# Kernel optimization log

Hardware: AMD Instinct MI355X
Metric: run time of the kernel (lower is better)

## Reference

```python
import jax, jax.numpy as jnp
import numpy as np

EPS_COS = 1e-8   # torch cosine_similarity denominator clamp
EPS_W = 1e-6     # min-max normalization epsilon from the module


def setup_inputs() -> dict:
    key = jax.random.key(0)
    k1, k2, k3 = jax.random.split(key, 3)
    N, D = 4096, 512
    return {
        "image_features": jax.random.normal(k1, (N, D), dtype=jnp.float32),
        "text_features": jax.random.normal(k2, (N, D), dtype=jnp.float32),
        "instr_d": jax.random.randint(k3, (N,), 0, 64, dtype=jnp.int64),
    }


def reference(image_features, text_features, instr_d):
    text_features = jax.lax.stop_gradient(text_features)  # .detach() in original
    N = image_features.shape[0]

    # per-row min-max normalized text-text similarity -> per-pair margins
    text_sim = jnp.einsum('id,jd->ij', text_features, text_features)  # [N,N]
    mn = jnp.min(text_sim, axis=1, keepdims=True)
    mx = jnp.max(text_sim, axis=1, keepdims=True)
    text_weights = (text_sim - mn) / (mx - mn + EPS_W)

    # pairwise cosine similarity image[i] vs text[j]
    img_norm = jnp.linalg.norm(image_features, axis=1)   # [N]
    txt_norm = jnp.linalg.norm(text_features, axis=1)    # [N]
    dots = jnp.einsum('id,jd->ij', image_features, text_features)
    cos = dots / jnp.maximum(img_norm[:, None] * txt_norm[None, :], EPS_COS)

    # aligned if i == j or same instruction id
    aligned = (instr_d[:, None] == instr_d[None, :]) | jnp.eye(N, dtype=bool)

    # cosine_embedding_loss: y=1 -> 1-cos ; y=-1 -> max(0, cos - margin)
    per_pair = jnp.where(aligned, 1.0 - cos, jnp.maximum(0.0, cos - text_weights))
    return jnp.mean(per_pair)
```

## Files before the change

kernel.cpp:

```cpp
#include <hip/hip_runtime.h>
#include <stdint.h>

#define NROWS 4096
#define DIM   512
#define EPS_W   1e-6f
#define NT    (NROWS / 128)
#define NKS   (DIM / 64)
#define NS    528

typedef unsigned short ushort_t;
typedef __attribute__((ext_vector_type(8))) short   short8;
typedef __attribute__((ext_vector_type(8))) unsigned short ushort8;
typedef __attribute__((ext_vector_type(4))) float   floatx4;

__device__ inline ushort_t f2bf(float x) {
    unsigned u = __float_as_uint(x);
    unsigned r = (u + 0x7FFFu + ((u >> 16) & 1u)) >> 16;
    return (ushort_t)r;
}
__device__ inline float bf2f(ushort_t u) {
    return __uint_as_float(((unsigned)u) << 16);
}
__device__ inline unsigned fmap(float f) {
    unsigned u = __float_as_uint(f);
    return (u & 0x80000000u) ? ~u : (u | 0x80000000u);
}
__device__ inline float funmap(unsigned u) {
    return __uint_as_float((u & 0x80000000u) ? (u & 0x7fffffffu) : ~u);
}

__device__ inline void gload_lds16(const void* g, void* l) {
    auto* gp = reinterpret_cast<const __attribute__((address_space(1))) unsigned int*>(
        reinterpret_cast<uintptr_t>(g));
    auto* lp = reinterpret_cast<__attribute__((address_space(3))) unsigned int*>(
        reinterpret_cast<uintptr_t>(l));
    __builtin_amdgcn_global_load_lds(gp, lp, 16, 0, 0);
}

__device__ inline void stage_tile(const ushort_t* __restrict__ gbase,
                                  ushort_t* lds, int wave, int lane) {
#pragma unroll
    for (int q = 0; q < 4; q++) {
        int row0 = wave * 32 + q * 8;
        int lrow = row0 + (lane >> 3);
        int src_chunk = (lane & 7) ^ (lane >> 3);
        const ushort_t* g = gbase + (size_t)lrow * DIM + src_chunk * 8;
        gload_lds16(g, lds + row0 * 64);
    }
}
__device__ inline short8 read_frag(const ushort_t* tile, int frag_row, int kk, int lane) {
    int r = frag_row * 16 + (lane & 15);
    int c = (kk * 4 + (lane >> 4)) ^ (lane & 7);
    return *reinterpret_cast<const short8*>(tile + r * 64 + c * 8);
}

__global__ __launch_bounds__(256) void prep_kernel(
    const float* __restrict__ img, const float* __restrict__ txt,
    ushort_t* __restrict__ Inrm, ushort_t* __restrict__ Traw,
    ushort_t* __restrict__ Tnrm,
    unsigned* __restrict__ mn_u, unsigned* __restrict__ mx_u) {
    const int wave = threadIdx.x >> 6, lane = threadIdx.x & 63;
    const int row = blockIdx.x * 4 + wave;
    const int col0 = lane * 8;
    {
        const float4* p = reinterpret_cast<const float4*>(img + (size_t)row * DIM + col0);
        float4 a = p[0], b = p[1];
        float ss = a.x*a.x + a.y*a.y + a.z*a.z + a.w*a.w
                 + b.x*b.x + b.y*b.y + b.z*b.z + b.w*b.w;
#pragma unroll
        for (int s = 1; s < 64; s <<= 1) ss += __shfl_xor(ss, s);
        float rin = rsqrtf(ss);
        ushort8 o;
        o[0]=f2bf(a.x*rin); o[1]=f2bf(a.y*rin); o[2]=f2bf(a.z*rin); o[3]=f2bf(a.w*rin);
        o[4]=f2bf(b.x*rin); o[5]=f2bf(b.y*rin); o[6]=f2bf(b.z*rin); o[7]=f2bf(b.w*rin);
        *reinterpret_cast<ushort8*>(Inrm + (size_t)row * DIM + col0) = o;
    }
    {
        const float4* p = reinterpret_cast<const float4*>(txt + (size_t)row * DIM + col0);
        float4 a = p[0], b = p[1];
        float ss = a.x*a.x + a.y*a.y + a.z*a.z + a.w*a.w
                 + b.x*b.x + b.y*b.y + b.z*b.z + b.w*b.w;
#pragma unroll
        for (int s = 1; s < 64; s <<= 1) ss += __shfl_xor(ss, s);
        float rtn = rsqrtf(ss);
        ushort8 r8, n8;
        r8[0]=f2bf(a.x); r8[1]=f2bf(a.y); r8[2]=f2bf(a.z); r8[3]=f2bf(a.w);
        r8[4]=f2bf(b.x); r8[5]=f2bf(b.y); r8[6]=f2bf(b.z); r8[7]=f2bf(b.w);
        n8[0]=f2bf(a.x*rtn); n8[1]=f2bf(a.y*rtn); n8[2]=f2bf(a.z*rtn); n8[3]=f2bf(a.w*rtn);
        n8[4]=f2bf(b.x*rtn); n8[5]=f2bf(b.y*rtn); n8[6]=f2bf(b.z*rtn); n8[7]=f2bf(b.w*rtn);
        *reinterpret_cast<ushort8*>(Traw + (size_t)row * DIM + col0) = r8;
        *reinterpret_cast<ushort8*>(Tnrm + (size_t)row * DIM + col0) = n8;
    }
    if (lane == 0) { mn_u[row] = 0xFFFFFFFFu; mx_u[row] = 0u; }
}

template <int SONLY>
__global__ __launch_bounds__(256) void gemm_kernel(
    const ushort_t* __restrict__ Traw, const ushort_t* __restrict__ Inrm,
    const ushort_t* __restrict__ Tnrm,
    unsigned* __restrict__ mn_u, unsigned* __restrict__ mx_u,
    ushort_t* __restrict__ simbuf, ushort_t* __restrict__ dotbuf) {
    __shared__ __align__(16) ushort_t LB[32768];
    ushort_t* TaB = LB;
    ushort_t* TbB = LB + 16384;
    int type, ti, tj;
    if (SONLY) {
        type = 0; ti = (int)blockIdx.x >> 5; tj = (int)blockIdx.x & 31;
    } else {
        int bid = (int)blockIdx.x;
        if (bid < NS) {
            type = 0;
            int u = bid;
            int t = (int)(32.5f - sqrtf(32.5f * 32.5f - 2.0f * (float)u));
            int off = 32 * t - (t * (t - 1)) / 2;
            if (off > u) { t--; off = 32 * t - (t * (t - 1)) / 2; }
            else if (off + (32 - t) <= u) { off += (32 - t); t++; }
            ti = t; tj = t + (u - off);
        } else {
            type = 1; int v = bid - NS; ti = v >> 5; tj = v & 31;
        }
    }
    const int wave = threadIdx.x >> 6, lane = threadIdx.x & 63;
    const int wr = wave >> 1, wc = wave & 1;
    const ushort_t* gA = (type ? Inrm : Traw) + (size_t)(ti * 128) * DIM;
    const ushort_t* gB = (type ? Tnrm : Traw) + (size_t)(tj * 128) * DIM;

    floatx4 acc[4][4];
#pragma unroll
    for (int m = 0; m < 4; m++)
#pragma unroll
        for (int n = 0; n < 4; n++) acc[m][n] = (floatx4){0.f, 0.f, 0.f, 0.f};

    stage_tile(gA, TaB, wave, lane);
    stage_tile(gB, TbB, wave, lane);
    __syncthreads();
#pragma unroll
    for (int t = 0; t < NKS; t++) {
        if (t + 1 < NKS) {
            stage_tile(gA + (t + 1) * 64, TaB + ((t + 1) & 1) * 8192, wave, lane);
            stage_tile(gB + (t + 1) * 64, TbB + ((t + 1) & 1) * 8192, wave, lane);
        }
#pragma unroll
        for (int kk = 0; kk < 2; kk++) {
            short8 a[4], b[4];
#pragma unroll
            for (int m = 0; m < 4; m++) a[m] = read_frag(TaB + (t & 1) * 8192, wr * 4 + m, kk, lane);
#pragma unroll
            for (int n = 0; n < 4; n++) b[n] = read_frag(TbB + (t & 1) * 8192, wc * 4 + n, kk, lane);
#pragma unroll
            for (int m = 0; m < 4; m++)
#pragma unroll
                for (int n = 0; n < 4; n++)
                    acc[m][n] = __builtin_amdgcn_mfma_f32_16x16x32_bf16(a[m], b[n], acc[m][n], 0, 0, 0);
        }
        __syncthreads();
    }

    ushort_t* sp = (type ? dotbuf : simbuf)
                 + ((size_t)((ti * NT + tj) * 4 + wave)) * 4096;

    if (type == 0) {
#pragma unroll
        for (int m = 0; m < 4; m++) {
#pragma unroll
            for (int reg = 0; reg < 4; reg++) {
                float vmin = acc[m][0][reg], vmax = acc[m][0][reg];
#pragma unroll
                for (int n = 1; n < 4; n++) {
                    vmin = fminf(vmin, acc[m][n][reg]);
                    vmax = fmaxf(vmax, acc[m][n][reg]);
                }
#pragma unroll
                for (int s = 1; s < 16; s <<= 1) {
                    vmin = fminf(vmin, __shfl_xor(vmin, s));
                    vmax = fmaxf(vmax, __shfl_xor(vmax, s));
                }
                if ((lane & 15) == 0) {
                    int row_g = ti * 128 + wr * 64 + m * 16 + (lane >> 4) * 4 + reg;
                    atomicMin(&mn_u[row_g], fmap(vmin));
                    atomicMax(&mx_u[row_g], fmap(vmax));
                }
            }
        }
        if (!SONLY && ti != tj) {
#pragma unroll
            for (int n = 0; n < 4; n++) {
                float cmin = acc[0][n][0], cmax = acc[0][n][0];
#pragma unroll
                for (int m = 0; m < 4; m++)
#pragma unroll
                    for (int reg = 0; reg < 4; reg++) {
                        float v = acc[m][n][reg];
                        cmin = fminf(cmin, v); cmax = fmaxf(cmax, v);
                    }
                cmin = fminf(cmin, __shfl_xor(cmin, 16));
                cmax = fmaxf(cmax, __shfl_xor(cmax, 16));
                cmin = fminf(cmin, __shfl_xor(cmin, 32));
                cmax = fmaxf(cmax, __shfl_xor(cmax, 32));
                if ((lane >> 4) == 0) {
                    int row_g = tj * 128 + wc * 64 + n * 16 + lane;
                    atomicMin(&mn_u[row_g], fmap(cmin));
                    atomicMax(&mx_u[row_g], fmap(cmax));
                }
            }
        }
    }
#pragma unroll
    for (int c = 0; c < 8; c++) {
        int m = c >> 1, n0 = (c & 1) * 2;
        ushort8 o;
        o[0] = f2bf(acc[m][n0][0]);     o[1] = f2bf(acc[m][n0][1]);
        o[2] = f2bf(acc[m][n0][2]);     o[3] = f2bf(acc[m][n0][3]);
        o[4] = f2bf(acc[m][n0 + 1][0]); o[5] = f2bf(acc[m][n0 + 1][1]);
        o[6] = f2bf(acc[m][n0 + 1][2]); o[7] = f2bf(acc[m][n0 + 1][3]);
        *reinterpret_cast<ushort8*>(sp + c * 512 + lane * 8) = o;
    }

    if (!SONLY && type == 0 && ti != tj) {
        const int rb0 = wr * 64, cb0 = wc * 64;
        const int l4 = lane >> 4, l15 = lane & 15;
#pragma unroll
        for (int m = 0; m < 4; m++)
#pragma unroll
            for (int n = 0; n < 4; n++)
#pragma unroll
                for (int reg = 0; reg < 4; reg++)
                    LB[(rb0 + m * 16 + l4 * 4 + reg) * 132 + (cb0 + n * 16 + l15)]
                        = f2bf(acc[m][n][reg]);
        __syncthreads();
        ushort_t* sp2 = simbuf + ((size_t)((tj * NT + ti) * 4 + wave)) * 4096;
#pragma unroll
        for (int cc = 0; cc < 8; cc++) {
            int m = cc >> 1, n0 = (cc & 1) * 2;
            int rw0 = (wave >> 1) * 64 + m * 16 + l4 * 4;
            ushort8 o;
#pragma unroll
            for (int h = 0; h < 2; h++) {
                int cw = (wave & 1) * 64 + (n0 + h) * 16 + l15;
                ushort4 v4 = *reinterpret_cast<const ushort4*>(&LB[cw * 132 + rw0]);
                o[h * 4 + 0] = v4.x; o[h * 4 + 1] = v4.y;
                o[h * 4 + 2] = v4.z; o[h * 4 + 3] = v4.w;
            }
            *reinterpret_cast<ushort8*>(sp2 + cc * 512 + lane * 8) = o;
        }
    }
}

__global__ __launch_bounds__(256) void params_kernel(
    const unsigned* __restrict__ mn_u, const unsigned* __restrict__ mx_u,
    float2* __restrict__ params2) {
    int i = blockIdx.x * 256 + threadIdx.x;
    float mn = funmap(mn_u[i]), mx = funmap(mx_u[i]);
    params2[i] = make_float2(mn, 1.0f / (mx - mn + EPS_W));
}

__global__ __launch_bounds__(256) void loss_kernel(
    const ushort_t* __restrict__ simbuf, const ushort_t* __restrict__ dotbuf,
    const float2* __restrict__ params2, const int* __restrict__ instr,
    float* __restrict__ out) {
    __shared__ float red[4];
    const int t = blockIdx.x * 256 + threadIdx.x;
    ushort8 sv[8], dv[8];
#pragma unroll
    for (int k = 0; k < 8; k++) {
        int s = t + k * 262144;
        sv[k] = __builtin_nontemporal_load(
            reinterpret_cast<const ushort8*>(simbuf + (size_t)s * 8));
        dv[k] = __builtin_nontemporal_load(
            reinterpret_cast<const ushort8*>(dotbuf + (size_t)s * 8));
    }
    const int wtid0 = t >> 9;
    const int r = t & 511;
    const int c = r >> 6, ln = r & 63;
    const int wv0 = wtid0 & 3, tj = (wtid0 >> 2) & 31;
    const int ti0 = wtid0 >> 7;
    const int m = c >> 1, n0 = (c & 1) * 2;
    const int rb_lo = (wv0 >> 1) * 64 + m * 16 + (ln >> 4) * 4;
    const int cb = tj * 128 + (wv0 & 1) * 64 + (ln & 15);
    const int ic0 = instr[cb + n0 * 16];
    const int ic1 = instr[cb + n0 * 16 + 16];
    const int col0g = cb + n0 * 16, col1g = col0g + 16;

    float lsum = 0.f;
#pragma unroll
    for (int k = 0; k < 8; k++) {
        int rb = (ti0 + 4 * k) * 128 + rb_lo;
        float4 pA = *reinterpret_cast<const float4*>(params2 + rb);
        float4 pB = *reinterpret_cast<const float4*>(params2 + rb + 2);
        int4  ir4 = *reinterpret_cast<const int4*>(instr + rb);
#pragma unroll
        for (int e = 0; e < 8; e++) {
            const int reg = e & 3, hn = e >> 2;
            float mn, wvv; int ir;
            if (reg == 0)      { mn = pA.x; wvv = pA.y; ir = ir4.x; }
            else if (reg == 1) { mn = pA.z; wvv = pA.w; ir = ir4.y; }
            else if (reg == 2) { mn = pB.x; wvv = pB.y; ir = ir4.z; }
            else               { mn = pB.z; wvv = pB.w; ir = ir4.w; }
            int ic = hn ? ic1 : ic0;
            int row = rb + reg, col = hn ? col1g : col0g;
            float cosv = bf2f(dv[k][e]);
            float w = (bf2f(sv[k][e]) - mn) * wvv;
            bool aligned = (ir == ic) || (row == col);
            lsum += aligned ? (1.0f - cosv) : fmaxf(0.0f, cosv - w);
        }
    }
#pragma unroll
    for (int s = 1; s < 64; s <<= 1) lsum += __shfl_xor(lsum, s);
    const int wave = threadIdx.x >> 6, lane = threadIdx.x & 63;
    if (lane == 0) red[wave] = lsum;
    __syncthreads();
    if (threadIdx.x == 0) {
        float v = red[0] + red[1] + red[2] + red[3];
        atomicAdd(out, v * (1.0f / ((float)NROWS * (float)NROWS)));
    }
}

__global__ __launch_bounds__(256) void dloss_kernel(
    const ushort_t* __restrict__ Inrm, const ushort_t* __restrict__ Tnrm,
    const float2* __restrict__ params2, const int* __restrict__ instr,
    const ushort_t* __restrict__ simbuf, float* __restrict__ out) {
    __shared__ __align__(16) ushort_t Ta[2][128 * 64];
    __shared__ __align__(16) ushort_t Tb[2][128 * 64];
    const int b2 = blockIdx.x;
    const int ti = b2 >> 5, tj = b2 & 31;
    const int wave = threadIdx.x >> 6, lane = threadIdx.x & 63;
    const int wr = wave >> 1, wc = wave & 1;
    const ushort_t* gA = Inrm + (size_t)(ti * 128) * DIM;
    const ushort_t* gB = Tnrm + (size_t)(tj * 128) * DIM;

    floatx4 acc[4][4];
#pragma unroll
    for (int m = 0; m < 4; m++)
#pragma unroll
        for (int n = 0; n < 4; n++) acc[m][n] = (floatx4){0.f, 0.f, 0.f, 0.f};

    stage_tile(gA, Ta[0], wave, lane);
    stage_tile(gB, Tb[0], wave, lane);
    __syncthreads();
#pragma unroll
    for (int t = 0; t < NKS; t++) {
        if (t + 1 < NKS) {
            stage_tile(gA + (t + 1) * 64, Ta[(t + 1) & 1], wave, lane);
            stage_tile(gB + (t + 1) * 64, Tb[(t + 1) & 1], wave, lane);
        }
#pragma unroll
        for (int kk = 0; kk < 2; kk++) {
            short8 a[4], b[4];
#pragma unroll
            for (int m = 0; m < 4; m++) a[m] = read_frag(Ta[t & 1], wr * 4 + m, kk, lane);
#pragma unroll
            for (int n = 0; n < 4; n++) b[n] = read_frag(Tb[t & 1], wc * 4 + n, kk, lane);
#pragma unroll
            for (int m = 0; m < 4; m++)
#pragma unroll
                for (int n = 0; n < 4; n++)
                    acc[m][n] = __builtin_amdgcn_mfma_f32_16x16x32_bf16(a[m], b[n], acc[m][n], 0, 0, 0);
        }
        __syncthreads();
    }

    const ushort_t* sp = simbuf + ((size_t)((ti * NT + tj) * 4 + wave)) * 4096;
    const int rbase0 = ti * 128 + wr * 64;
    const int cbase0 = tj * 128 + wc * 64;
    int ic4[4];
#pragma unroll
    for (int n = 0; n < 4; n++) ic4[n] = instr[cbase0 + n * 16 + (lane & 15)];
    float lsum = 0.f;
#pragma unroll
    for (int m = 0; m < 4; m++) {
        ushort8 s0 = *reinterpret_cast<const ushort8*>(sp + (m * 2 + 0) * 512 + lane * 8);
        ushort8 s1 = *reinterpret_cast<const ushort8*>(sp + (m * 2 + 1) * 512 + lane * 8);
        int rb = rbase0 + m * 16 + (lane >> 4) * 4;
#pragma unroll
        for (int reg = 0; reg < 4; reg++) {
            int row_g = rb + reg;
            float2 pp = params2[row_g];
            int   ir  = instr[row_g];
#pragma unroll
            for (int n = 0; n < 4; n++) {
                int col_g = cbase0 + n * 16 + (lane & 15);
                float simv = (n < 2) ? bf2f(s0[(n & 1) * 4 + reg])
                                     : bf2f(s1[(n & 1) * 4 + reg]);
                float cosv = acc[m][n][reg];
                float w = (simv - pp.x) * pp.y;
                bool aligned = (ir == ic4[n]) || (row_g == col_g);
                lsum += aligned ? (1.0f - cosv) : fmaxf(0.0f, cosv - w);
            }
        }
    }
#pragma unroll
    for (int s = 1; s < 64; s <<= 1) lsum += __shfl_xor(lsum, s);
    if (lane == 0)
        atomicAdd(out, lsum * (1.0f / ((float)NROWS * (float)NROWS)));
}

extern "C" void kernel_launch(void* const* d_in, const int* in_sizes, int n_in,
                              void* d_out, int out_size, void* d_ws, size_t ws_size,
                              hipStream_t stream) {
    const float* img = (const float*)d_in[0];
    const float* txt = (const float*)d_in[1];
    const int* instr = (const int*)d_in[2];
    float* out = (float*)d_out;

    char* ws = (char*)d_ws;
    const size_t MAT = (size_t)NROWS * DIM * 2;
    ushort_t* Traw = (ushort_t*)ws;
    ushort_t* Inrm = (ushort_t*)(ws + MAT);
    ushort_t* Tnrm = (ushort_t*)(ws + 2 * MAT);
    unsigned* mn_u = (unsigned*)(ws + 3 * MAT);
    unsigned* mx_u = mn_u + NROWS;
    float2* params2 = (float2*)(mx_u + NROWS);
    ushort_t* simbuf = (ushort_t*)(params2 + NROWS);
    ushort_t* dotbuf = simbuf + (size_t)NROWS * NROWS;
    const size_t need = 3 * MAT + (size_t)NROWS * 16
                      + 2 * (size_t)NROWS * NROWS * 2;

    hipMemsetAsync(d_out, 0, sizeof(float), stream);
    prep_kernel<<<NROWS / 4, 256, 0, stream>>>(img, txt, Inrm, Traw, Tnrm, mn_u, mx_u);
    if (ws_size >= need) {
        gemm_kernel<0><<<NS + NT * NT, 256, 0, stream>>>(Traw, Inrm, Tnrm,
                                                         mn_u, mx_u, simbuf, dotbuf);
        params_kernel<<<NROWS / 256, 256, 0, stream>>>(mn_u, mx_u, params2);
        loss_kernel<<<1024, 256, 0, stream>>>(simbuf, dotbuf, params2, instr, out);
    } else {
        gemm_kernel<1><<<NT * NT, 256, 0, stream>>>(Traw, Inrm, Tnrm,
                                                    mn_u, mx_u, simbuf, simbuf);
        params_kernel<<<NROWS / 256, 256, 0, stream>>>(mn_u, mx_u, params2);
        dloss_kernel<<<NT * NT, 256, 0, stream>>>(Inrm, Tnrm, params2, instr, simbuf, out);
    }
}
```

Measured before the change: 83.08 us.

## Halve GEMM K-tile to shrink LDS and double loss kernel grid

The GEMM kernels now stage K-slices of 32 instead of 64, with a new XOR swizzle and read pattern. This cuts shared memory from 64KB to about 34KB per block so more blocks can be resident per CU, at the cost of twice as many barrier-separated iterations. A barrier is added before the epilogue reuses LDS for the transpose. The loss kernel launches twice as many blocks, each doing half the loads, and switches from nontemporal loads to plain ones.

```diff
diff --git a/kernel.cpp b/kernel.cpp
--- a/kernel.cpp
+++ b/kernel.cpp
@@ -5,7 +5,7 @@
 #define DIM   512
 #define EPS_W   1e-6f
 #define NT    (NROWS / 128)
-#define NKS   (DIM / 64)
+#define NKS32 16
 #define NS    528
 
 typedef unsigned short ushort_t;
@@ -37,21 +37,20 @@
     __builtin_amdgcn_global_load_lds(gp, lp, 16, 0, 0);
 }
 
-__device__ inline void stage_tile(const ushort_t* __restrict__ gbase,
-                                  ushort_t* lds, int wave, int lane) {
-#pragma unroll
-    for (int q = 0; q < 4; q++) {
-        int row0 = wave * 32 + q * 8;
-        int lrow = row0 + (lane >> 3);
-        int src_chunk = (lane & 7) ^ (lane >> 3);
-        const ushort_t* g = gbase + (size_t)lrow * DIM + src_chunk * 8;
-        gload_lds16(g, lds + row0 * 64);
-    }
-}
-__device__ inline short8 read_frag(const ushort_t* tile, int frag_row, int kk, int lane) {
-    int r = frag_row * 16 + (lane & 15);
-    int c = (kk * 4 + (lane >> 4)) ^ (lane & 7);
-    return *reinterpret_cast<const short8*>(tile + r * 64 + c * 8);
+__device__ inline void stage32(const ushort_t* __restrict__ gbase,
+                               ushort_t* lds, int wave, int lane) {
+#pragma unroll
+    for (int q = 0; q < 2; q++) {
+        int row0 = wave * 32 + q * 16;
+        int row = row0 + (lane >> 2);
+        int gchunk = (lane & 3) ^ ((lane >> 3) & 3);
+        gload_lds16(gbase + (size_t)row * DIM + gchunk * 8, lds + row0 * 32);
+    }
+}
+__device__ inline short8 read_frag32(const ushort_t* tile, int fr, int lane) {
+    int r = fr * 16 + (lane & 15);
+    int p = (lane >> 4) ^ ((r >> 1) & 3);
+    return *reinterpret_cast<const short8*>(tile + r * 32 + p * 8);
 }
 
 __global__ __launch_bounds__(256) void prep_kernel(
@@ -100,9 +99,7 @@
     const ushort_t* __restrict__ Tnrm,
     unsigned* __restrict__ mn_u, unsigned* __restrict__ mx_u,
     ushort_t* __restrict__ simbuf, ushort_t* __restrict__ dotbuf) {
-    __shared__ __align__(16) ushort_t LB[32768];
-    ushort_t* TaB = LB;
-    ushort_t* TbB = LB + 16384;
+    __shared__ __align__(16) ushort_t LB[17408];
     int type, ti, tj;
     if (SONLY) {
         type = 0; ti = (int)blockIdx.x >> 5; tj = (int)blockIdx.x & 31;
@@ -131,28 +128,25 @@
 #pragma unroll
         for (int n = 0; n < 4; n++) acc[m][n] = (floatx4){0.f, 0.f, 0.f, 0.f};
 
-    stage_tile(gA, TaB, wave, lane);
-    stage_tile(gB, TbB, wave, lane);
+    stage32(gA, LB, wave, lane);
+    stage32(gB, LB + 8192, wave, lane);
     __syncthreads();
 #pragma unroll
-    for (int t = 0; t < NKS; t++) {
-        if (t + 1 < NKS) {
-            stage_tile(gA + (t + 1) * 64, TaB + ((t + 1) & 1) * 8192, wave, lane);
-            stage_tile(gB + (t + 1) * 64, TbB + ((t + 1) & 1) * 8192, wave, lane);
-        }
-#pragma unroll
-        for (int kk = 0; kk < 2; kk++) {
-            short8 a[4], b[4];
-#pragma unroll
-            for (int m = 0; m < 4; m++) a[m] = read_frag(TaB + (t & 1) * 8192, wr * 4 + m, kk, lane);
-#pragma unroll
-            for (int n = 0; n < 4; n++) b[n] = read_frag(TbB + (t & 1) * 8192, wc * 4 + n, kk, lane);
-#pragma unroll
-            for (int m = 0; m < 4; m++)
-#pragma unroll
-                for (int n = 0; n < 4; n++)
-                    acc[m][n] = __builtin_amdgcn_mfma_f32_16x16x32_bf16(a[m], b[n], acc[m][n], 0, 0, 0);
-        }
+    for (int t = 0; t < NKS32; t++) {
+        if (t + 1 < NKS32) {
+            stage32(gA + (t + 1) * 32, LB + ((t + 1) & 1) * 4096, wave, lane);
+            stage32(gB + (t + 1) * 32, LB + 8192 + ((t + 1) & 1) * 4096, wave, lane);
+        }
+        short8 a[4], b[4];
+#pragma unroll
+        for (int m = 0; m < 4; m++) a[m] = read_frag32(LB + (t & 1) * 4096, wr * 4 + m, lane);
+#pragma unroll
+        for (int n = 0; n < 4; n++) b[n] = read_frag32(LB + 8192 + (t & 1) * 4096, wc * 4 + n, lane);
+#pragma unroll
+        for (int m = 0; m < 4; m++)
+#pragma unroll
+            for (int n = 0; n < 4; n++)
+                acc[m][n] = __builtin_amdgcn_mfma_f32_16x16x32_bf16(a[m], b[n], acc[m][n], 0, 0, 0);
         __syncthreads();
     }
 
@@ -219,6 +213,7 @@
     if (!SONLY && type == 0 && ti != tj) {
         const int rb0 = wr * 64, cb0 = wc * 64;
         const int l4 = lane >> 4, l15 = lane & 15;
+        __syncthreads();
 #pragma unroll
         for (int m = 0; m < 4; m++)
 #pragma unroll
@@ -260,14 +255,12 @@
     float* __restrict__ out) {
     __shared__ float red[4];
     const int t = blockIdx.x * 256 + threadIdx.x;
-    ushort8 sv[8], dv[8];
-#pragma unroll
-    for (int k = 0; k < 8; k++) {
-        int s = t + k * 262144;
-        sv[k] = __builtin_nontemporal_load(
-            reinterpret_cast<const ushort8*>(simbuf + (size_t)s * 8));
-        dv[k] = __builtin_nontemporal_load(
-            reinterpret_cast<const ushort8*>(dotbuf + (size_t)s * 8));
+    ushort8 sv[4], dv[4];
+#pragma unroll
+    for (int k = 0; k < 4; k++) {
+        int s = t + k * 524288;
+        sv[k] = *reinterpret_cast<const ushort8*>(simbuf + (size_t)s * 8);
+        dv[k] = *reinterpret_cast<const ushort8*>(dotbuf + (size_t)s * 8);
     }
     const int wtid0 = t >> 9;
     const int r = t & 511;
@@ -283,8 +276,8 @@
 
     float lsum = 0.f;
 #pragma unroll
-    for (int k = 0; k < 8; k++) {
-        int rb = (ti0 + 4 * k) * 128 + rb_lo;
+    for (int k = 0; k < 4; k++) {
+        int rb = (ti0 + 8 * k) * 128 + rb_lo;
         float4 pA = *reinterpret_cast<const float4*>(params2 + rb);
         float4 pB = *reinterpret_cast<const float4*>(params2 + rb + 2);
         int4  ir4 = *reinterpret_cast<const int4*>(instr + rb);
@@ -319,8 +312,7 @@
     const ushort_t* __restrict__ Inrm, const ushort_t* __restrict__ Tnrm,
     const float2* __restrict__ params2, const int* __restrict__ instr,
     const ushort_t* __restrict__ simbuf, float* __restrict__ out) {
-    __shared__ __align__(16) ushort_t Ta[2][128 * 64];
-    __shared__ __align__(16) ushort_t Tb[2][128 * 64];
+    __shared__ __align__(16) ushort_t LB[16384];
     const int b2 = blockIdx.x;
     const int ti = b2 >> 5, tj = b2 & 31;
     const int wave = threadIdx.x >> 6, lane = threadIdx.x & 63;
@@ -334,28 +326,25 @@
 #pragma unroll
         for (int n = 0; n < 4; n++) acc[m][n] = (floatx4){0.f, 0.f, 0.f, 0.f};
 
-    stage_tile(gA, Ta[0], wave, lane);
-    stage_tile(gB, Tb[0], wave, lane);
+    stage32(gA, LB, wave, lane);
+    stage32(gB, LB + 8192, wave, lane);
     __syncthreads();
 #pragma unroll
-    for (int t = 0; t < NKS; t++) {
-        if (t + 1 < NKS) {
-            stage_tile(gA + (t + 1) * 64, Ta[(t + 1) & 1], wave, lane);
-            stage_tile(gB + (t + 1) * 64, Tb[(t + 1) & 1], wave, lane);
-        }
-#pragma unroll
-        for (int kk = 0; kk < 2; kk++) {
-            short8 a[4], b[4];
-#pragma unroll
-            for (int m = 0; m < 4; m++) a[m] = read_frag(Ta[t & 1], wr * 4 + m, kk, lane);
-#pragma unroll
-            for (int n = 0; n < 4; n++) b[n] = read_frag(Tb[t & 1], wc * 4 + n, kk, lane);
-#pragma unroll
-            for (int m = 0; m < 4; m++)
-#pragma unroll
-                for (int n = 0; n < 4; n++)
-                    acc[m][n] = __builtin_amdgcn_mfma_f32_16x16x32_bf16(a[m], b[n], acc[m][n], 0, 0, 0);
-        }
+    for (int t = 0; t < NKS32; t++) {
+        if (t + 1 < NKS32) {
+            stage32(gA + (t + 1) * 32, LB + ((t + 1) & 1) * 4096, wave, lane);
+            stage32(gB + (t + 1) * 32, LB + 8192 + ((t + 1) & 1) * 4096, wave, lane);
+        }
+        short8 a[4], b[4];
+#pragma unroll
+        for (int m = 0; m < 4; m++) a[m] = read_frag32(LB + (t & 1) * 4096, wr * 4 + m, lane);
+#pragma unroll
+        for (int n = 0; n < 4; n++) b[n] = read_frag32(LB + 8192 + (t & 1) * 4096, wc * 4 + n, lane);
+#pragma unroll
+        for (int m = 0; m < 4; m++)
+#pragma unroll
+            for (int n = 0; n < 4; n++)
+                acc[m][n] = __builtin_amdgcn_mfma_f32_16x16x32_bf16(a[m], b[n], acc[m][n], 0, 0, 0);
         __syncthreads();
     }
 
@@ -421,7 +410,7 @@
         gemm_kernel<0><<<NS + NT * NT, 256, 0, stream>>>(Traw, Inrm, Tnrm,
                                                          mn_u, mx_u, simbuf, dotbuf);
         params_kernel<<<NROWS / 256, 256, 0, stream>>>(mn_u, mx_u, params2);
-        loss_kernel<<<1024, 256, 0, stream>>>(simbuf, dotbuf, params2, instr, out);
+        loss_kernel<<<2048, 256, 0, stream>>>(simbuf, dotbuf, params2, instr, out);
     } else {
         gemm_kernel<1><<<NT * NT, 256, 0, stream>>>(Traw, Inrm, Tnrm,
                                                     mn_u, mx_u, simbuf, simbuf);
```

Result: slower. 94.37 us (+13.6%).
